# Optimization experiments

Measured on AMD Instinct MI355X. Metric: run time of the kernel, lower is better.

## Reference

```python
import jax, jax.numpy as jnp
import numpy as np
from itertools import combinations

BASIS = 16  # identity + sums over every nonempty subset of the 4 set axes


def eq4_layer(x, coefs, bias):
    """Permutation-equivariant 4->4 set layer.
    x: (B, Din, n, n, n, n); coefs: (Din, Dout, 16); bias: (Dout,)
    Basis op 0 is identity; ops 1..15 are sums over each nonempty subset of the
    four set axes, broadcast back to full shape. We never stack the 16 full-size
    ops: pooled ops are contracted in their small (keepdims) form and broadcast-added.
    """
    out = jnp.einsum('ds,bdijkl->bsijkl', coefs[:, :, 0], x)
    b = 1
    for r in range(1, 5):
        for axes in combinations((2, 3, 4, 5), r):
            m = x.sum(axis=axes, keepdims=True)  # small marginal tensor
            out = out + jnp.einsum('ds,bd...->bs...', coefs[:, :, b], m)
            b += 1
    return out + bias.reshape(1, -1, 1, 1, 1, 1)


def setup_inputs() -> dict:
    key = jax.random.key(0)
    ks = jax.random.split(key, 9)
    B, n = 4, 24
    nembed, embed_dim, hid, out_dim = 1000, 15, 16, 16
    D = embed_dim + 1  # 16, = layers[0]
    s = 0.1
    return {
        'xcat': jax.random.randint(ks[0], (B, n), 0, nembed),
        'xfeat': jax.random.normal(ks[1], (B, n), dtype=jnp.float32),
        'embed': jax.random.normal(ks[2], (nembed, embed_dim), dtype=jnp.float32) * s,
        'coefs1': jax.random.normal(ks[3], (D, hid, BASIS), dtype=jnp.float32) * s,
        'bias1': jnp.zeros((hid,), dtype=jnp.float32),
        'coefs2': jax.random.normal(ks[4], (hid, out_dim, BASIS), dtype=jnp.float32) * s,
        'bias2': jnp.zeros((out_dim,), dtype=jnp.float32),
        'w_out': jax.random.normal(ks[5], (1, out_dim), dtype=jnp.float32) * s,
        'b_out': jnp.zeros((1,), dtype=jnp.float32),
    }


def reference(xcat, xfeat, embed, coefs1, bias1, coefs2, bias2, w_out, b_out):
    e = jax.nn.relu(embed[xcat])                       # (B, n, embed_dim)
    x = jnp.concatenate([e, xfeat[..., None]], axis=-1)  # (B, n, D)
    # 4th-order outer product per channel: (B, D, n, n, n, n)
    T = jnp.einsum('bid,bjd,bkd,bld->bdijkl', x, x, x, x)
    T = jax.nn.relu(eq4_layer(T, coefs1, bias1))
    T = jax.nn.relu(eq4_layer(T, coefs2, bias2))
    pooled = T.sum(axis=(2, 3, 4, 5))                  # (B, out_dim)
    return pooled @ w_out.T + b_out                    # (B, 1)
```

## Files before the change

### kernel.cpp

```cpp
#include <hip/hip_runtime.h>
#include <hip/hip_bf16.h>


#define NB 4
#define NN 24
#define ND 16
#define NS 16
#define NO 16
#define NKL 576
#define TSTRIDE 1152

typedef unsigned int u32;
typedef unsigned short u16;

__device__ __forceinline__ u16 f2bf(float f) {
  u32 u = __float_as_uint(f);
  u = (u + 0x7fffu + ((u >> 16) & 1u)) >> 16;
  return (u16)u;
}
__device__ __forceinline__ float bflo(u32 u) { return __uint_as_float(u << 16); }
__device__ __forceinline__ float bfhi(u32 u) { return __uint_as_float(u & 0xffff0000u); }

__global__ __launch_bounds__(192, 2) void kb_eval(
    const int* __restrict__ xcat, const float* __restrict__ xfeat,
    const float* __restrict__ embed,
    const float* __restrict__ coefs1, const float* __restrict__ bias1,
    const float* __restrict__ coefs2,
    u32* __restrict__ T1g, u32* __restrict__ mkc_p, u32* __restrict__ mlc_p,
    u32* __restrict__ mklc_p) {
  const int blk = blockIdx.x;
  const int j = blk % NN, i = (blk / NN) % NN, b = blk / (NN * NN);
  const int t = threadIdx.x;
  __shared__ float sx[NN * ND];
  __shared__ float SwL[16];
  __shared__ float Af[256], tb[256], tg[256], td[256];
  __shared__ float dconst[16];
  __shared__ __align__(16) float tabL[TSTRIDE];
  __shared__ u32 T1p[NKL][9];
  __shared__ __align__(16) float rk[NN][20], rl[NN][20];
  __shared__ __align__(16) float rkl[16];
  __shared__ __align__(16) float c2kT[16][20], c2lT[16][20], c2qT[16][20];

  for (int idx = t; idx < NN * ND; idx += 192) {
    int d = idx & 15, ii = idx >> 4;
    float v;
    if (d < 15) v = fmaxf(embed[xcat[b * NN + ii] * 15 + d], 0.f);
    else        v = xfeat[b * NN + ii];
    sx[idx] = v;
  }
  for (int idx = t; idx < 256; idx += 192) {
    int s = idx >> 4, s2 = idx & 15;
    c2kT[s2][s] = coefs2[idx * 16 + 3];
    c2lT[s2][s] = coefs2[idx * 16 + 4];
    c2qT[s2][s] = coefs2[idx * 16 + 10];
  }
  __syncthreads();
  if (t < 16) {
    float s = 0.f;
    for (int ii = 0; ii < NN; ++ii) s += sx[ii * 16 + t];
    SwL[t] = s;
  }
  __syncthreads();
  for (int idx = t; idx < 256; idx += 192) {
    int d = idx >> 4, s = idx & 15;
    const float* c = coefs1 + idx * 16;
    float xi = sx[i * 16 + d], xj = sx[j * 16 + d];
    float Sv = SwL[d];
    float S2 = Sv * Sv, S3 = S2 * Sv, S4 = S2 * S2, pij = xi * xj;
    Af[s * 16 + d] = c[0] * pij + c[1] * Sv * xj + c[2] * Sv * xi + c[5] * S2;
    tb[idx] = c[4] * Sv * pij + c[9] * S2 * xi + c[7] * S2 * xj + c[12] * S3;
    tg[idx] = c[3] * Sv * pij + c[8] * S2 * xi + c[6] * S2 * xj + c[11] * S3;
    td[idx] = c[10] * S2 * pij + c[14] * S3 * xi + c[13] * S3 * xj + c[15] * S4;
  }
  __syncthreads();
  if (t < 16) {
    float sd = 0.f;
    for (int d = 0; d < 16; ++d) sd += td[d * 16 + t];
    dconst[t] = sd + bias1[t];
  }
  __syncthreads();
  if (t < 128) {
    int s = t >> 3, m = t & 7;
    tabL[t] = __uint_as_float((u32)f2bf(Af[s * 16 + 2 * m]) |
                              ((u32)f2bf(Af[s * 16 + 2 * m + 1]) << 16));
  }
  for (int idx = t; idx < 768; idx += 192) {
    int pos = idx >> 4, s = idx & 15;
    if (pos < NN) {
      float acc = 0.f;
#pragma unroll
      for (int d = 0; d < 16; ++d) acc += tb[d * 16 + s] * sx[pos * 16 + d];
      tabL[128 + s * 32 + (pos / 3) * 4 + pos % 3] = acc;
    } else {
      int l = pos - NN;
      float acc = dconst[s];
#pragma unroll
      for (int d = 0; d < 16; ++d) acc += tg[d * 16 + s] * sx[l * 16 + d];
      tabL[640 + s * 32 + (l / 3) * 4 + l % 3] = acc;
    }
  }
  __syncthreads();

  const int grp = t >> 3, sub = t & 7, vr = 3 * sub;
  const int grpPos = (grp / 3) * 4 + grp % 3;
  float P0[16], P1[16], P2[16];
#pragma unroll
  for (int d = 0; d < 16; ++d) {
    float xc = sx[grp * 16 + d];
    P0[d] = sx[vr * 16 + d] * xc;
    P1[d] = sx[(vr + 1) * 16 + d] * xc;
    P2[d] = sx[(vr + 2) * 16 + d] * xc;
  }
  float pr0[16], pr1[16], pr2[16];
#pragma unroll
  for (int s = 0; s < 16; ++s) {
    const uint4* ap = (const uint4*)(tabL + s * 8);
    uint4 A0 = ap[0], A1 = ap[1];
    u32 qa[8] = {A0.x, A0.y, A0.z, A0.w, A1.x, A1.y, A1.z, A1.w};
    float Afr[16];
#pragma unroll
    for (int m = 0; m < 8; ++m) {
      Afr[2 * m] = bflo(qa[m]);
      Afr[2 * m + 1] = bfhi(qa[m]);
    }
    float4 vb4 = *(const float4*)(tabL + 128 + s * 32 + sub * 4);
    float ct = tabL[640 + s * 32 + grpPos];
    float v0 = vb4.x + ct, v1 = vb4.y + ct, v2 = vb4.z + ct;
#pragma unroll
    for (int d = 0; d < 16; ++d) {
      v0 += Afr[d] * P0[d];
      v1 += Afr[d] * P1[d];
      v2 += Afr[d] * P2[d];
    }
    pr0[s] = fmaxf(v0, 0.f);
    pr1[s] = fmaxf(v1, 0.f);
    pr2[s] = fmaxf(v2, 0.f);
  }
  const int klA = vr * NN + grp;
  auto emit = [&](float (&pr)[16], int kl) {
    u32 w[8];
#pragma unroll
    for (int m = 0; m < 8; ++m) {
      w[m] = (u32)f2bf(pr[2 * m]) | ((u32)f2bf(pr[2 * m + 1]) << 16);
      T1p[kl][m] = w[m];
    }
    uint4* gp = (uint4*)(T1g + ((size_t)blk * NKL + kl) * 8);
    gp[0] = make_uint4(w[0], w[1], w[2], w[3]);
    gp[1] = make_uint4(w[4], w[5], w[6], w[7]);
  };
  emit(pr0, klA); emit(pr1, klA + NN); emit(pr2, klA + 2 * NN);
  __syncthreads();

  for (int idx = t; idx < NN * NS; idx += 192) {
    int a = idx >> 4, s = idx & 15, m = s >> 1;
    u32 odd = (u32)(s & 1);
    float sk = 0.f, sl = 0.f;
    for (int c = 0; c < NN; ++c) {
      u32 uk = T1p[c * NN + a][m];
      u32 ul = T1p[a * NN + c][m];
      sk += odd ? bfhi(uk) : bflo(uk);
      sl += odd ? bfhi(ul) : bflo(ul);
    }
    rk[a][s] = sk;
    rl[a][s] = sl;
  }
  __syncthreads();
  if (t < 16) {
    float v = 0.f;
    for (int a = 0; a < NN; ++a) v += rk[a][t];
    rkl[t] = v;
  }
  __syncthreads();
  for (int idx = t; idx < 392; idx += 192) {
    int m = idx & 7, pos = idx >> 3;
    const float* raw; const float (*cT)[20]; u32* dst;
    if (pos < NN)           { raw = rk[pos];      cT = c2kT; dst = mkc_p + ((size_t)blk * NN + pos) * 8 + m; }
    else if (pos < 2 * NN)  { raw = rl[pos - NN]; cT = c2lT; dst = mlc_p + ((size_t)blk * NN + (pos - NN)) * 8 + m; }
    else                    { raw = rkl;          cT = c2qT; dst = mklc_p + (size_t)blk * 8 + m; }
    float o0 = 0.f, o1 = 0.f;
#pragma unroll
    for (int w = 0; w < 4; ++w) {
      float4 rv = ((const float4*)raw)[w];
      float4 m0 = ((const float4*)(&cT[2 * m][0]))[w];
      float4 m1 = ((const float4*)(&cT[2 * m + 1][0]))[w];
      o0 += rv.x * m0.x + rv.y * m0.y + rv.z * m0.z + rv.w * m0.w;
      o1 += rv.x * m1.x + rv.y * m1.y + rv.z * m1.z + rv.w * m1.w;
    }
    *dst = (u32)f2bf(o0) | ((u32)f2bf(o1) << 16);
  }
}

__global__ __launch_bounds__(256) void k3_marg(
    const u32* __restrict__ T1g, const float* __restrict__ coefs2,
    u32* __restrict__ mi_p, u32* __restrict__ mj_p,
    u32* __restrict__ mic_p, u32* __restrict__ mjc_p,
    float* __restrict__ quad_part) {
  const int t = threadIdx.x, bb = blockIdx.x;
  const int pos = bb * 256 + t;
  const bool isI = pos < 55296;
  const int p = isI ? pos : pos - 55296;
  __shared__ __align__(16) float ccT[16][20];
  __shared__ float qred[4][16];
  {
    int s = t >> 4, s2 = t & 15;
    ccT[s2][s] = coefs2[t * 16 + (isI ? 1 : 2)];
  }
  __syncthreads();
  const int ba = p / NKL, kl = p % NKL;
  const int b = ba / NN, a = ba % NN;
  const u32* base; size_t stride;
  if (isI) { base = T1g + ((size_t)(b * NN * NN + a) * NKL + kl) * 8; stride = (size_t)NN * NKL * 8; }
  else     { base = T1g + ((size_t)((b * NN + a) * NN) * NKL + kl) * 8; stride = (size_t)NKL * 8; }
  float raw[16];
#pragma unroll
  for (int s = 0; s < 16; ++s) raw[s] = 0.f;
  for (int c = 0; c < NN; ++c) {
    const uint4* q = (const uint4*)(base + c * stride);
    uint4 q0 = q[0], q1 = q[1];
    u32 qa[8] = {q0.x, q0.y, q0.z, q0.w, q1.x, q1.y, q1.z, q1.w};
#pragma unroll
    for (int m = 0; m < 8; ++m) {
      raw[2 * m] += bflo(qa[m]);
      raw[2 * m + 1] += bfhi(qa[m]);
    }
  }
  u32 rp[8], op[8];
#pragma unroll
  for (int m = 0; m < 8; ++m) {
    rp[m] = (u32)f2bf(raw[2 * m]) | ((u32)f2bf(raw[2 * m + 1]) << 16);
    float o0 = 0.f, o1 = 0.f;
#pragma unroll
    for (int w = 0; w < 4; ++w) {
      float4 m0 = ((const float4*)(&ccT[2 * m][0]))[w];
      float4 m1 = ((const float4*)(&ccT[2 * m + 1][0]))[w];
      o0 += m0.x * raw[4 * w] + m0.y * raw[4 * w + 1] + m0.z * raw[4 * w + 2] + m0.w * raw[4 * w + 3];
      o1 += m1.x * raw[4 * w] + m1.y * raw[4 * w + 1] + m1.z * raw[4 * w + 2] + m1.w * raw[4 * w + 3];
    }
    op[m] = (u32)f2bf(o0) | ((u32)f2bf(o1) << 16);
  }
  uint4* rdst = (uint4*)((isI ? mi_p : mj_p) + (size_t)p * 8);
  rdst[0] = make_uint4(rp[0], rp[1], rp[2], rp[3]);
  rdst[1] = make_uint4(rp[4], rp[5], rp[6], rp[7]);
  uint4* cdst = (uint4*)((isI ? mic_p : mjc_p) + (size_t)p * 8);
  cdst[0] = make_uint4(op[0], op[1], op[2], op[3]);
  cdst[1] = make_uint4(op[4], op[5], op[6], op[7]);
  if (isI) {
#pragma unroll
    for (int s = 0; s < 16; ++s) {
      float v = raw[s];
      for (int off = 32; off; off >>= 1) v += __shfl_xor(v, off, 64);
      raw[s] = v;
    }
    if ((t & 63) == 0) {
      int w = t >> 6;
#pragma unroll
      for (int s = 0; s < 16; ++s) qred[w][s] = raw[s];
    }
  }
  __syncthreads();
  if (isI && t < 16)
    quad_part[bb * 16 + t] = qred[0][t] + qred[1][t] + qred[2][t] + qred[3][t];
}

__global__ __launch_bounds__(256) void kd_derived(
    const u32* __restrict__ mi_p, const u32* __restrict__ mj_p,
    const float* __restrict__ quad_part, const float* __restrict__ coefs2,
    float* __restrict__ mijc, float* __restrict__ mikc, float* __restrict__ milc,
    float* __restrict__ mjkc, float* __restrict__ mjlc,
    float* __restrict__ mijkc, float* __restrict__ mijlc,
    float* __restrict__ miklc, float* __restrict__ mjklc,
    float* __restrict__ mijklc) {
  const int bb = blockIdx.x, t = threadIdx.x;
  __shared__ float cc[256];
  __shared__ float ex[32][17];
  __shared__ float tot[16];
  __shared__ float qr[64];
  if (bb < 360) {
    int tbl = bb / 72;
    cc[t] = coefs2[t * 16 + 5 + tbl];
    int pp = t >> 3, m = t & 7;
    int pos = (bb % 72) * 32 + pp;
    int b = pos / 576, rem = pos % 576;
    const u32* srcb; int stride;
    if (tbl == 0) { srcb = mi_p + ((size_t)b * 24 * 576 + rem) * 8 + m; stride = 576 * 8; }
    else if (tbl == 1) { int jj = rem / 24, l = rem % 24;
      srcb = mi_p + (((size_t)(b * 24 + jj)) * 576 + l) * 8 + m; stride = 24 * 8; }
    else if (tbl == 2) { int jj = rem / 24, k = rem % 24;
      srcb = mi_p + (((size_t)(b * 24 + jj)) * 576 + k * 24) * 8 + m; stride = 8; }
    else if (tbl == 3) { int ii = rem / 24, l = rem % 24;
      srcb = mj_p + (((size_t)(b * 24 + ii)) * 576 + l) * 8 + m; stride = 24 * 8; }
    else { int ii = rem / 24, k = rem % 24;
      srcb = mj_p + (((size_t)(b * 24 + ii)) * 576 + k * 24) * 8 + m; stride = 8; }
    float v0 = 0.f, v1 = 0.f;
#pragma unroll 4
    for (int x = 0; x < 24; ++x) {
      u32 u = srcb[(size_t)x * stride];
      v0 += bflo(u); v1 += bfhi(u);
    }
    ex[pp][2 * m] = v0;
    ex[pp][2 * m + 1] = v1;
    __syncthreads();
    float* dst = (tbl == 0 ? mijc : tbl == 1 ? mikc : tbl == 2 ? milc : tbl == 3 ? mjkc : mjlc);
    for (int idx = t; idx < 512; idx += 256) {
      int pp2 = idx >> 4, s2 = idx & 15;
      float o = 0.f;
#pragma unroll
      for (int ss = 0; ss < 16; ++ss) o += cc[ss * 16 + s2] * ex[pp2][ss];
      dst[(size_t)((bb % 72) * 32 + pp2) * 16 + s2] = o;
    }
    return;
  }
  if (bb < 360 + 384) {
    int idx = bb - 360;
    int tbl = idx / 96, rr = idx % 96;
    int b = rr / 24, a = rr % 24;
    cc[t] = coefs2[t * 16 + 11 + tbl];
    int gg = t >> 3, m = t & 7;
    const u32* src = (tbl == 3 ? mj_p : mi_p);
    float v0 = 0.f, v1 = 0.f;
#pragma unroll 2
    for (int it = 0; it < 18; ++it) {
      int u = gg + (it << 5);
      size_t addr;
      if (tbl == 0) { int j = u / 24, k = u % 24;
        addr = (((size_t)(b * 24 + j)) * 576 + k * 24 + a) * 8 + m; }
      else if (tbl == 1) { int j = u / 24, l = u % 24;
        addr = (((size_t)(b * 24 + j)) * 576 + a * 24 + l) * 8 + m; }
      else {
        addr = (((size_t)(b * 24 + a)) * 576 + u) * 8 + m; }
      u32 uu = src[addr];
      v0 += bflo(uu); v1 += bfhi(uu);
    }
    ex[gg][2 * m] = v0;
    ex[gg][2 * m + 1] = v1;
    __syncthreads();
    if (t < 16) {
      float w2 = 0.f;
#pragma unroll
      for (int g2 = 0; g2 < 32; ++g2) w2 += ex[g2][t];
      tot[t] = w2;
    }
    __syncthreads();
    if (t < 16) {
      float o = 0.f;
#pragma unroll
      for (int ss = 0; ss < 16; ++ss) o += cc[ss * 16 + t] * tot[ss];
      float* dst = (tbl == 0 ? mijkc : tbl == 1 ? mijlc : tbl == 2 ? miklc : mjklc);
      dst[(size_t)(b * 24 + a) * 16 + t] = o;
    }
    return;
  }
  if (t < 64) {
    int b = t >> 4, s = t & 15;
    float v = 0.f;
    for (int c = 0; c < 54; ++c) v += quad_part[(b * 54 + c) * 16 + s];
    qr[t] = v;
  }
  __syncthreads();
  if (t < 64) {
    int b = t >> 4, s2 = t & 15;
    float o = 0.f;
#pragma unroll
    for (int s = 0; s < 16; ++s) o += coefs2[(s * 16 + s2) * 16 + 15] * qr[b * 16 + s];
    mijklc[t] = o;
  }
}

__global__ __launch_bounds__(192, 2) void k5_final(
    const u32* __restrict__ T1g,
    const u32* __restrict__ mic_p, const u32* __restrict__ mjc_p,
    const u32* __restrict__ mkc_p, const u32* __restrict__ mlc_p,
    const u32* __restrict__ mklc_p,
    const float* __restrict__ mijc, const float* __restrict__ mikc,
    const float* __restrict__ milc, const float* __restrict__ mjkc,
    const float* __restrict__ mjlc,
    const float* __restrict__ mijkc, const float* __restrict__ mijlc,
    const float* __restrict__ miklc, const float* __restrict__ mjklc,
    const float* __restrict__ mijklc,
    const float* __restrict__ coefs2, const float* __restrict__ bias2,
    const float* __restrict__ w_out, float* __restrict__ pool_part) {
  const int orig = blockIdx.x;
  const int blk = (orig & 7) * 288 + (orig >> 3);
  const int j = blk % NN, i2 = (blk / NN) % NN, b = blk / (NN * NN);
  const int t = threadIdx.x;
  __shared__ __align__(16) u32 c2p[128];
  __shared__ __align__(16) float Kt[NN][16], Lt[NN][16];
  __shared__ __align__(16) float cterm[16], wl[16];
  __shared__ float wsum[3];

  if (t < 128) {
    int s = t >> 3, m = t & 7;
    c2p[t] = (u32)f2bf(coefs2[(s * 16 + 2 * m) * 16]) |
             ((u32)f2bf(coefs2[(s * 16 + 2 * m + 1) * 16]) << 16);
  }
  for (int idx = t; idx < NN * NO; idx += 192) {
    int kk = idx >> 4, s2 = idx & 15, m = s2 >> 1;
    u32 odd = (u32)(s2 & 1);
    u32 ul = mlc_p[((size_t)blk * NN + kk) * 8 + m];
    u32 uk = mkc_p[((size_t)blk * NN + kk) * 8 + m];
    Kt[kk][s2] = (odd ? bfhi(ul) : bflo(ul))
               + mjlc[(size_t)((b * NN + i2) * NN + kk) * NS + s2]
               + milc[(size_t)((b * NN + j) * NN + kk) * NS + s2]
               + mijlc[(size_t)(b * NN + kk) * NS + s2];
    Lt[kk][s2] = (odd ? bfhi(uk) : bflo(uk))
               + mjkc[(size_t)((b * NN + i2) * NN + kk) * NS + s2]
               + mikc[(size_t)((b * NN + j) * NN + kk) * NS + s2]
               + mijkc[(size_t)(b * NN + kk) * NS + s2];
  }
  if (t < NO) {
    u32 uq = mklc_p[(size_t)blk * 8 + (t >> 1)];
    cterm[t] = ((t & 1) ? bfhi(uq) : bflo(uq))
             + miklc[(size_t)(b * NN + j) * NS + t]
             + mjklc[(size_t)(b * NN + i2) * NS + t]
             + mijklc[(size_t)b * NS + t] + bias2[t];
    wl[t] = w_out[t];
  }
  __syncthreads();

  u32 qa0[8], qa1[8], qa2[8];
  float acc0[16], acc1[16], acc2[16];
  auto loadElem = [&](int c, u32 (&qa)[8], float (&acc)[16]) {
    const int kl = t + 192 * c;
    const int k = kl / NN, l = kl % NN;
    const uint4* pt = (const uint4*)(T1g + ((size_t)blk * NKL + kl) * 8);
    const uint4* pi = (const uint4*)(mic_p + ((size_t)((b * NN + j) * NKL + kl)) * 8);
    const uint4* pj = (const uint4*)(mjc_p + ((size_t)((b * NN + i2) * NKL + kl)) * 8);
    const float4* ps = (const float4*)(mijc + ((size_t)(b * NKL + kl)) * 16);
    uint4 t0 = pt[0], t1 = pt[1];
    uint4 i0 = pi[0], i1 = pi[1];
    uint4 j0 = pj[0], j1 = pj[1];
    float4 s0 = ps[0], s1 = ps[1], s2v = ps[2], s3 = ps[3];
    qa[0] = t0.x; qa[1] = t0.y; qa[2] = t0.z; qa[3] = t0.w;
    qa[4] = t1.x; qa[5] = t1.y; qa[6] = t1.z; qa[7] = t1.w;
    u32 ia[8] = {i0.x, i0.y, i0.z, i0.w, i1.x, i1.y, i1.z, i1.w};
    u32 ja[8] = {j0.x, j0.y, j0.z, j0.w, j1.x, j1.y, j1.z, j1.w};
    float sv[16];
    ((float4*)sv)[0] = s0; ((float4*)sv)[1] = s1; ((float4*)sv)[2] = s2v; ((float4*)sv)[3] = s3;
#pragma unroll
    for (int m = 0; m < 8; ++m) {
      acc[2 * m]     = cterm[2 * m]     + Kt[k][2 * m]     + Lt[l][2 * m]
                     + bflo(ia[m]) + bflo(ja[m]) + sv[2 * m];
      acc[2 * m + 1] = cterm[2 * m + 1] + Kt[k][2 * m + 1] + Lt[l][2 * m + 1]
                     + bfhi(ia[m]) + bfhi(ja[m]) + sv[2 * m + 1];
    }
  };
  loadElem(0, qa0, acc0); loadElem(1, qa1, acc1); loadElem(2, qa2, acc2);

#pragma unroll
  for (int s = 0; s < 16; ++s) {
    const uint4* cp = (const uint4*)(c2p + s * 8);
    uint4 C0 = cp[0], C1 = cp[1];
    u32 ca[8] = {C0.x, C0.y, C0.z, C0.w, C1.x, C1.y, C1.z, C1.w};
    float row[16];
#pragma unroll
    for (int m = 0; m < 8; ++m) {
      row[2 * m] = bflo(ca[m]);
      row[2 * m + 1] = bfhi(ca[m]);
    }
    float v0 = (s & 1) ? bfhi(qa0[s >> 1]) : bflo(qa0[s >> 1]);
    float v1 = (s & 1) ? bfhi(qa1[s >> 1]) : bflo(qa1[s >> 1]);
    float v2 = (s & 1) ? bfhi(qa2[s >> 1]) : bflo(qa2[s >> 1]);
#pragma unroll
    for (int s2 = 0; s2 < 16; ++s2) {
      acc0[s2] += row[s2] * v0;
      acc1[s2] += row[s2] * v1;
      acc2[s2] += row[s2] * v2;
    }
  }
  float p = 0.f;
#pragma unroll
  for (int s2 = 0; s2 < 16; ++s2)
    p += wl[s2] * (fmaxf(acc0[s2], 0.f) + fmaxf(acc1[s2], 0.f) + fmaxf(acc2[s2], 0.f));
  for (int off = 32; off; off >>= 1) p += __shfl_down(p, off, 64);
  if ((t & 63) == 0) wsum[t >> 6] = p;
  __syncthreads();
  if (t == 0) pool_part[blk] = wsum[0] + wsum[1] + wsum[2];
}

__global__ __launch_bounds__(256) void k6_out(
    const float* __restrict__ pool_part, const float* __restrict__ b_out,
    float* __restrict__ out) {
  const int t = threadIdx.x;
  const int b = t >> 6, lane = t & 63;
  float v = 0.f;
  for (int c = lane; c < 576; c += 64) v += pool_part[b * 576 + c];
  for (int off = 32; off; off >>= 1) v += __shfl_down(v, off, 64);
  if (lane == 0) out[b] = v + b_out[0];
}

extern "C" void kernel_launch(void* const* d_in, const int* in_sizes, int n_in,
                              void* d_out, int out_size, void* d_ws, size_t ws_size,
                              hipStream_t stream) {
  (void)in_sizes; (void)n_in; (void)out_size; (void)ws_size;
  const int*   xcat   = (const int*)d_in[0];
  const float* xfeat  = (const float*)d_in[1];
  const float* embed  = (const float*)d_in[2];
  const float* coefs1 = (const float*)d_in[3];
  const float* bias1  = (const float*)d_in[4];
  const float* coefs2 = (const float*)d_in[5];
  const float* bias2  = (const float*)d_in[6];
  const float* w_out  = (const float*)d_in[7];
  const float* b_out  = (const float*)d_in[8];
  float* out = (float*)d_out;
  char* ws = (char*)d_ws;

  u32*   T1g      = (u32*)(ws + 0);
  u32*   mi_p     = (u32*)(ws + 42467328);
  u32*   mj_p     = (u32*)(ws + 44236800);
  u32*   mic_p    = (u32*)(ws + 46006272);
  u32*   mjc_p    = (u32*)(ws + 47775744);
  u32*   mkc_p    = (u32*)(ws + 49545216);
  u32*   mlc_p    = (u32*)(ws + 51314688);
  u32*   mklc_p   = (u32*)(ws + 53084160);
  float* mijc     = (float*)(ws + 53157888);
  float* mikc     = (float*)(ws + 53305344);
  float* milc     = (float*)(ws + 53452800);
  float* mjkc     = (float*)(ws + 53600256);
  float* mjlc     = (float*)(ws + 53747712);
  float* mijkc    = (float*)(ws + 53895168);
  float* mijlc    = (float*)(ws + 53901312);
  float* miklc    = (float*)(ws + 53907456);
  float* mjklc    = (float*)(ws + 53913600);
  float* mijklc   = (float*)(ws + 53919744);
  float* quad_part= (float*)(ws + 53920000);
  float* pool_part= (float*)(ws + 53933824);

  kb_eval<<<NB * NN * NN, 192, 0, stream>>>(xcat, xfeat, embed, coefs1, bias1,
                                            coefs2, T1g, mkc_p, mlc_p, mklc_p);
  k3_marg<<<432, 256, 0, stream>>>(T1g, coefs2, mi_p, mj_p, mic_p, mjc_p, quad_part);
  kd_derived<<<745, 256, 0, stream>>>(mi_p, mj_p, quad_part, coefs2,
                                      mijc, mikc, milc, mjkc, mjlc,
                                      mijkc, mijlc, miklc, mjklc, mijklc);
  k5_final<<<NB * NN * NN, 192, 0, stream>>>(T1g, mic_p, mjc_p, mkc_p, mlc_p, mklc_p,
                                             mijc, mikc, milc, mjkc, mjlc,
                                             mijkc, mijlc, miklc, mjklc, mijklc,
                                             coefs2, bias2, w_out, pool_part);
  k6_out<<<1, 256, 0, stream>>>(pool_part, b_out, out);
}
```

Baseline: 101.3 us.

## Move per-block k/l marginal reductions from kb_eval into k5_final

The k- and l-axis marginal sums of T1, and their contraction with coefs2, now happen in k5_final instead of kb_eval. k5_final already loads the block's T1 tile, so the mkc/mlc/mklc intermediate buffers and their global writes and reads disappear. kb_eval becomes lighter: fewer shared arrays, fewer barriers, the A table computed straight from coefs1, the dconst reduction folded into the tg loop, and T1 packed to bf16 on the fly. This moves reduction work, shared memory and barriers into k5_final, which may lower its occupancy. It also adds an unroll pragma in k3_marg.

```diff
diff --git a/kernel.cpp b/kernel.cpp
--- a/kernel.cpp
+++ b/kernel.cpp
@@ -8,7 +8,6 @@
 #define NS 16
 #define NO 16
 #define NKL 576
-#define TSTRIDE 1152
 
 typedef unsigned int u32;
 typedef unsigned short u16;
@@ -25,21 +24,14 @@
     const int* __restrict__ xcat, const float* __restrict__ xfeat,
     const float* __restrict__ embed,
     const float* __restrict__ coefs1, const float* __restrict__ bias1,
-    const float* __restrict__ coefs2,
-    u32* __restrict__ T1g, u32* __restrict__ mkc_p, u32* __restrict__ mlc_p,
-    u32* __restrict__ mklc_p) {
+    u32* __restrict__ T1g) {
   const int blk = blockIdx.x;
   const int j = blk % NN, i = (blk / NN) % NN, b = blk / (NN * NN);
   const int t = threadIdx.x;
   __shared__ float sx[NN * ND];
   __shared__ float SwL[16];
-  __shared__ float Af[256], tb[256], tg[256], td[256];
-  __shared__ float dconst[16];
-  __shared__ __align__(16) float tabL[TSTRIDE];
-  __shared__ u32 T1p[NKL][9];
-  __shared__ __align__(16) float rk[NN][20], rl[NN][20];
-  __shared__ __align__(16) float rkl[16];
-  __shared__ __align__(16) float c2kT[16][20], c2lT[16][20], c2qT[16][20];
+  __shared__ float tb[256], tg[256], td[256];
+  __shared__ __align__(16) float tabL[1152];
 
   for (int idx = t; idx < NN * ND; idx += 192) {
     int d = idx & 15, ii = idx >> 4;
@@ -48,12 +40,6 @@
     else        v = xfeat[b * NN + ii];
     sx[idx] = v;
   }
-  for (int idx = t; idx < 256; idx += 192) {
-    int s = idx >> 4, s2 = idx & 15;
-    c2kT[s2][s] = coefs2[idx * 16 + 3];
-    c2lT[s2][s] = coefs2[idx * 16 + 4];
-    c2qT[s2][s] = coefs2[idx * 16 + 10];
-  }
   __syncthreads();
   if (t < 16) {
     float s = 0.f;
@@ -67,23 +53,24 @@
     float xi = sx[i * 16 + d], xj = sx[j * 16 + d];
     float Sv = SwL[d];
     float S2 = Sv * Sv, S3 = S2 * Sv, S4 = S2 * S2, pij = xi * xj;
-    Af[s * 16 + d] = c[0] * pij + c[1] * Sv * xj + c[2] * Sv * xi + c[5] * S2;
     tb[idx] = c[4] * Sv * pij + c[9] * S2 * xi + c[7] * S2 * xj + c[12] * S3;
     tg[idx] = c[3] * Sv * pij + c[8] * S2 * xi + c[6] * S2 * xj + c[11] * S3;
     td[idx] = c[10] * S2 * pij + c[14] * S3 * xi + c[13] * S3 * xj + c[15] * S4;
   }
-  __syncthreads();
-  if (t < 16) {
-    float sd = 0.f;
-    for (int d = 0; d < 16; ++d) sd += td[d * 16 + t];
-    dconst[t] = sd + bias1[t];
-  }
-  __syncthreads();
   if (t < 128) {
     int s = t >> 3, m = t & 7;
-    tabL[t] = __uint_as_float((u32)f2bf(Af[s * 16 + 2 * m]) |
-                              ((u32)f2bf(Af[s * 16 + 2 * m + 1]) << 16));
-  }
+    float af[2];
+#pragma unroll
+    for (int h = 0; h < 2; ++h) {
+      int d = 2 * m + h;
+      const float* c = coefs1 + (d * 16 + s) * 16;
+      float xi = sx[i * 16 + d], xj = sx[j * 16 + d];
+      float Sv = SwL[d];
+      af[h] = c[0] * xi * xj + c[1] * Sv * xj + c[2] * Sv * xi + c[5] * Sv * Sv;
+    }
+    tabL[t] = __uint_as_float((u32)f2bf(af[0]) | ((u32)f2bf(af[1]) << 16));
+  }
+  __syncthreads();
   for (int idx = t; idx < 768; idx += 192) {
     int pos = idx >> 4, s = idx & 15;
     if (pos < NN) {
@@ -93,14 +80,14 @@
       tabL[128 + s * 32 + (pos / 3) * 4 + pos % 3] = acc;
     } else {
       int l = pos - NN;
-      float acc = dconst[s];
-#pragma unroll
-      for (int d = 0; d < 16; ++d) acc += tg[d * 16 + s] * sx[l * 16 + d];
+      float acc = bias1[s];
+#pragma unroll
+      for (int d = 0; d < 16; ++d)
+        acc += tg[d * 16 + s] * sx[l * 16 + d] + td[d * 16 + s];
       tabL[640 + s * 32 + (l / 3) * 4 + l % 3] = acc;
     }
   }
   __syncthreads();
-
   const int grp = t >> 3, sub = t & 7, vr = 3 * sub;
   const int grpPos = (grp / 3) * 4 + grp % 3;
   float P0[16], P1[16], P2[16];
@@ -111,7 +98,7 @@
     P1[d] = sx[(vr + 1) * 16 + d] * xc;
     P2[d] = sx[(vr + 2) * 16 + d] * xc;
   }
-  float pr0[16], pr1[16], pr2[16];
+  u32 w0[8], w1[8], w2[8];
 #pragma unroll
   for (int s = 0; s < 16; ++s) {
     const uint4* ap = (const uint4*)(tabL + s * 8);
@@ -132,62 +119,18 @@
       v1 += Afr[d] * P1[d];
       v2 += Afr[d] * P2[d];
     }
-    pr0[s] = fmaxf(v0, 0.f);
-    pr1[s] = fmaxf(v1, 0.f);
-    pr2[s] = fmaxf(v2, 0.f);
+    v0 = fmaxf(v0, 0.f); v1 = fmaxf(v1, 0.f); v2 = fmaxf(v2, 0.f);
+    u16 b0 = f2bf(v0), b1 = f2bf(v1), b2 = f2bf(v2);
+    if (s & 1) { w0[s >> 1] |= (u32)b0 << 16; w1[s >> 1] |= (u32)b1 << 16; w2[s >> 1] |= (u32)b2 << 16; }
+    else       { w0[s >> 1] = b0; w1[s >> 1] = b1; w2[s >> 1] = b2; }
   }
   const int klA = vr * NN + grp;
-  auto emit = [&](float (&pr)[16], int kl) {
-    u32 w[8];
-#pragma unroll
-    for (int m = 0; m < 8; ++m) {
-      w[m] = (u32)f2bf(pr[2 * m]) | ((u32)f2bf(pr[2 * m + 1]) << 16);
-      T1p[kl][m] = w[m];
-    }
+  auto emit = [&](u32 (&w)[8], int kl) {
     uint4* gp = (uint4*)(T1g + ((size_t)blk * NKL + kl) * 8);
     gp[0] = make_uint4(w[0], w[1], w[2], w[3]);
     gp[1] = make_uint4(w[4], w[5], w[6], w[7]);
   };
-  emit(pr0, klA); emit(pr1, klA + NN); emit(pr2, klA + 2 * NN);
-  __syncthreads();
-
-  for (int idx = t; idx < NN * NS; idx += 192) {
-    int a = idx >> 4, s = idx & 15, m = s >> 1;
-    u32 odd = (u32)(s & 1);
-    float sk = 0.f, sl = 0.f;
-    for (int c = 0; c < NN; ++c) {
-      u32 uk = T1p[c * NN + a][m];
-      u32 ul = T1p[a * NN + c][m];
-      sk += odd ? bfhi(uk) : bflo(uk);
-      sl += odd ? bfhi(ul) : bflo(ul);
-    }
-    rk[a][s] = sk;
-    rl[a][s] = sl;
-  }
-  __syncthreads();
-  if (t < 16) {
-    float v = 0.f;
-    for (int a = 0; a < NN; ++a) v += rk[a][t];
-    rkl[t] = v;
-  }
-  __syncthreads();
-  for (int idx = t; idx < 392; idx += 192) {
-    int m = idx & 7, pos = idx >> 3;
-    const float* raw; const float (*cT)[20]; u32* dst;
-    if (pos < NN)           { raw = rk[pos];      cT = c2kT; dst = mkc_p + ((size_t)blk * NN + pos) * 8 + m; }
-    else if (pos < 2 * NN)  { raw = rl[pos - NN]; cT = c2lT; dst = mlc_p + ((size_t)blk * NN + (pos - NN)) * 8 + m; }
-    else                    { raw = rkl;          cT = c2qT; dst = mklc_p + (size_t)blk * 8 + m; }
-    float o0 = 0.f, o1 = 0.f;
-#pragma unroll
-    for (int w = 0; w < 4; ++w) {
-      float4 rv = ((const float4*)raw)[w];
-      float4 m0 = ((const float4*)(&cT[2 * m][0]))[w];
-      float4 m1 = ((const float4*)(&cT[2 * m + 1][0]))[w];
-      o0 += rv.x * m0.x + rv.y * m0.y + rv.z * m0.z + rv.w * m0.w;
-      o1 += rv.x * m1.x + rv.y * m1.y + rv.z * m1.z + rv.w * m1.w;
-    }
-    *dst = (u32)f2bf(o0) | ((u32)f2bf(o1) << 16);
-  }
+  emit(w0, klA); emit(w1, klA + NN); emit(w2, klA + 2 * NN);
 }
 
 __global__ __launch_bounds__(256) void k3_marg(
@@ -214,6 +157,7 @@
   float raw[16];
 #pragma unroll
   for (int s = 0; s < 16; ++s) raw[s] = 0.f;
+#pragma unroll 4
   for (int c = 0; c < NN; ++c) {
     const uint4* q = (const uint4*)(base + c * stride);
     uint4 q0 = q[0], q1 = q[1];
@@ -369,8 +313,6 @@
 __global__ __launch_bounds__(192, 2) void k5_final(
     const u32* __restrict__ T1g,
     const u32* __restrict__ mic_p, const u32* __restrict__ mjc_p,
-    const u32* __restrict__ mkc_p, const u32* __restrict__ mlc_p,
-    const u32* __restrict__ mklc_p,
     const float* __restrict__ mijc, const float* __restrict__ mikc,
     const float* __restrict__ milc, const float* __restrict__ mjkc,
     const float* __restrict__ mjlc,
@@ -384,32 +326,85 @@
   const int j = blk % NN, i2 = (blk / NN) % NN, b = blk / (NN * NN);
   const int t = threadIdx.x;
   __shared__ __align__(16) u32 c2p[128];
+  __shared__ __align__(16) float c2kT[16][20], c2lT[16][20], c2qT[16][20];
+  __shared__ u32 T1p[NKL][9];
+  __shared__ __align__(16) float rk[NN][20], rl[NN][20];
+  __shared__ __align__(16) float rkl[16];
   __shared__ __align__(16) float Kt[NN][16], Lt[NN][16];
   __shared__ __align__(16) float cterm[16], wl[16];
   __shared__ float wsum[3];
 
+  u32 qa0[8], qa1[8], qa2[8];
+  auto loadT = [&](int c, u32 (&qa)[8]) {
+    const int kl = t + 192 * c;
+    const uint4* pt = (const uint4*)(T1g + ((size_t)blk * NKL + kl) * 8);
+    uint4 t0 = pt[0], t1 = pt[1];
+    qa[0] = t0.x; qa[1] = t0.y; qa[2] = t0.z; qa[3] = t0.w;
+    qa[4] = t1.x; qa[5] = t1.y; qa[6] = t1.z; qa[7] = t1.w;
+#pragma unroll
+    for (int m = 0; m < 8; ++m) T1p[kl][m] = qa[m];
+  };
+  loadT(0, qa0); loadT(1, qa1); loadT(2, qa2);
   if (t < 128) {
     int s = t >> 3, m = t & 7;
     c2p[t] = (u32)f2bf(coefs2[(s * 16 + 2 * m) * 16]) |
              ((u32)f2bf(coefs2[(s * 16 + 2 * m + 1) * 16]) << 16);
   }
+  for (int idx = t; idx < 256; idx += 192) {
+    int s = idx >> 4, s2 = idx & 15;
+    c2kT[s2][s] = coefs2[idx * 16 + 3];
+    c2lT[s2][s] = coefs2[idx * 16 + 4];
+    c2qT[s2][s] = coefs2[idx * 16 + 10];
+  }
+  __syncthreads();
+
+  for (int idx = t; idx < NN * NS; idx += 192) {
+    int a = idx >> 4, s = idx & 15, m = s >> 1;
+    u32 odd = (u32)(s & 1);
+    float sk = 0.f, sl = 0.f;
+    for (int c = 0; c < NN; ++c) {
+      u32 uk = T1p[c * NN + a][m];
+      u32 ul = T1p[a * NN + c][m];
+      sk += odd ? bfhi(uk) : bflo(uk);
+      sl += odd ? bfhi(ul) : bflo(ul);
+    }
+    rk[a][s] = sk;
+    rl[a][s] = sl;
+  }
+  __syncthreads();
+  if (t < 16) {
+    float v = 0.f;
+    for (int a = 0; a < NN; ++a) v += rk[a][t];
+    rkl[t] = v;
+  }
+  __syncthreads();
   for (int idx = t; idx < NN * NO; idx += 192) {
-    int kk = idx >> 4, s2 = idx & 15, m = s2 >> 1;
-    u32 odd = (u32)(s2 & 1);
-    u32 ul = mlc_p[((size_t)blk * NN + kk) * 8 + m];
-    u32 uk = mkc_p[((size_t)blk * NN + kk) * 8 + m];
-    Kt[kk][s2] = (odd ? bfhi(ul) : bflo(ul))
+    int kk = idx >> 4, s2 = idx & 15;
+    const float4* ck = (const float4*)(&c2kT[s2][0]);
+    const float4* cl = (const float4*)(&c2lT[s2][0]);
+    const float4* rkr = (const float4*)(&rk[kk][0]);
+    const float4* rlr = (const float4*)(&rl[kk][0]);
+    float ok = 0.f, ol = 0.f;
+#pragma unroll
+    for (int w = 0; w < 4; ++w) {
+      float4 mk4 = ck[w], ml4 = cl[w], rk4 = rkr[w], rl4 = rlr[w];
+      ok += mk4.x * rk4.x + mk4.y * rk4.y + mk4.z * rk4.z + mk4.w * rk4.w;
+      ol += ml4.x * rl4.x + ml4.y * rl4.y + ml4.z * rl4.z + ml4.w * rl4.w;
+    }
+    Lt[kk][s2] = ok
+               + mjkc[(size_t)((b * NN + i2) * NN + kk) * NS + s2]
+               + mikc[(size_t)((b * NN + j) * NN + kk) * NS + s2]
+               + mijkc[(size_t)(b * NN + kk) * NS + s2];
+    Kt[kk][s2] = ol
                + mjlc[(size_t)((b * NN + i2) * NN + kk) * NS + s2]
                + milc[(size_t)((b * NN + j) * NN + kk) * NS + s2]
                + mijlc[(size_t)(b * NN + kk) * NS + s2];
-    Lt[kk][s2] = (odd ? bfhi(uk) : bflo(uk))
-               + mjkc[(size_t)((b * NN + i2) * NN + kk) * NS + s2]
-               + mikc[(size_t)((b * NN + j) * NN + kk) * NS + s2]
-               + mijkc[(size_t)(b * NN + kk) * NS + s2];
   }
   if (t < NO) {
-    u32 uq = mklc_p[(size_t)blk * 8 + (t >> 1)];
-    cterm[t] = ((t & 1) ? bfhi(uq) : bflo(uq))
+    float oq = 0.f;
+#pragma unroll
+    for (int s = 0; s < 16; ++s) oq += c2qT[t][s] * rkl[s];
+    cterm[t] = oq
              + miklc[(size_t)(b * NN + j) * NS + t]
              + mjklc[(size_t)(b * NN + i2) * NS + t]
              + mijklc[(size_t)b * NS + t] + bias2[t];
@@ -417,21 +412,16 @@
   }
   __syncthreads();
 
-  u32 qa0[8], qa1[8], qa2[8];
   float acc0[16], acc1[16], acc2[16];
-  auto loadElem = [&](int c, u32 (&qa)[8], float (&acc)[16]) {
+  auto initElem = [&](int c, u32 (&qa)[8], float (&acc)[16]) {
     const int kl = t + 192 * c;
     const int k = kl / NN, l = kl % NN;
-    const uint4* pt = (const uint4*)(T1g + ((size_t)blk * NKL + kl) * 8);
     const uint4* pi = (const uint4*)(mic_p + ((size_t)((b * NN + j) * NKL + kl)) * 8);
     const uint4* pj = (const uint4*)(mjc_p + ((size_t)((b * NN + i2) * NKL + kl)) * 8);
     const float4* ps = (const float4*)(mijc + ((size_t)(b * NKL + kl)) * 16);
-    uint4 t0 = pt[0], t1 = pt[1];
     uint4 i0 = pi[0], i1 = pi[1];
     uint4 j0 = pj[0], j1 = pj[1];
     float4 s0 = ps[0], s1 = ps[1], s2v = ps[2], s3 = ps[3];
-    qa[0] = t0.x; qa[1] = t0.y; qa[2] = t0.z; qa[3] = t0.w;
-    qa[4] = t1.x; qa[5] = t1.y; qa[6] = t1.z; qa[7] = t1.w;
     u32 ia[8] = {i0.x, i0.y, i0.z, i0.w, i1.x, i1.y, i1.z, i1.w};
     u32 ja[8] = {j0.x, j0.y, j0.z, j0.w, j1.x, j1.y, j1.z, j1.w};
     float sv[16];
@@ -444,7 +434,7 @@
                      + bfhi(ia[m]) + bfhi(ja[m]) + sv[2 * m + 1];
     }
   };
-  loadElem(0, qa0, acc0); loadElem(1, qa1, acc1); loadElem(2, qa2, acc2);
+  initElem(0, qa0, acc0); initElem(1, qa1, acc1); initElem(2, qa2, acc2);
 
 #pragma unroll
   for (int s = 0; s < 16; ++s) {
@@ -509,29 +499,25 @@
   u32*   mj_p     = (u32*)(ws + 44236800);
   u32*   mic_p    = (u32*)(ws + 46006272);
   u32*   mjc_p    = (u32*)(ws + 47775744);
-  u32*   mkc_p    = (u32*)(ws + 49545216);
-  u32*   mlc_p    = (u32*)(ws + 51314688);
-  u32*   mklc_p   = (u32*)(ws + 53084160);
-  float* mijc     = (float*)(ws + 53157888);
-  float* mikc     = (float*)(ws + 53305344);
-  float* milc     = (float*)(ws + 53452800);
-  float* mjkc     = (float*)(ws + 53600256);
-  float* mjlc     = (float*)(ws + 53747712);
-  float* mijkc    = (float*)(ws + 53895168);
-  float* mijlc    = (float*)(ws + 53901312);
-  float* miklc    = (float*)(ws + 53907456);
-  float* mjklc    = (float*)(ws + 53913600);
-  float* mijklc   = (float*)(ws + 53919744);
-  float* quad_part= (float*)(ws + 53920000);
-  float* pool_part= (float*)(ws + 53933824);
-
-  kb_eval<<<NB * NN * NN, 192, 0, stream>>>(xcat, xfeat, embed, coefs1, bias1,
-                                            coefs2, T1g, mkc_p, mlc_p, mklc_p);
+  float* mijc     = (float*)(ws + 49545216);
+  float* mikc     = (float*)(ws + 49692672);
+  float* milc     = (float*)(ws + 49840128);
+  float* mjkc     = (float*)(ws + 49987584);
+  float* mjlc     = (float*)(ws + 50135040);
+  float* mijkc    = (float*)(ws + 50282496);
+  float* mijlc    = (float*)(ws + 50288640);
+  float* miklc    = (float*)(ws + 50294784);
+  float* mjklc    = (float*)(ws + 50300928);
+  float* mijklc   = (float*)(ws + 50307072);
+  float* quad_part= (float*)(ws + 50307328);
+  float* pool_part= (float*)(ws + 50321152);
+
+  kb_eval<<<NB * NN * NN, 192, 0, stream>>>(xcat, xfeat, embed, coefs1, bias1, T1g);
   k3_marg<<<432, 256, 0, stream>>>(T1g, coefs2, mi_p, mj_p, mic_p, mjc_p, quad_part);
   kd_derived<<<745, 256, 0, stream>>>(mi_p, mj_p, quad_part, coefs2,
                                       mijc, mikc, milc, mjkc, mjlc,
                                       mijkc, mijlc, miklc, mjklc, mijklc);
-  k5_final<<<NB * NN * NN, 192, 0, stream>>>(T1g, mic_p, mjc_p, mkc_p, mlc_p, mklc_p,
+  k5_final<<<NB * NN * NN, 192, 0, stream>>>(T1g, mic_p, mjc_p,
                                              mijc, mikc, milc, mjkc, mjlc,
                                              mijkc, mijlc, miklc, mjklc, mijklc,
                                              coefs2, bias2, w_out, pool_part);
```

After: 169.0 us. +66.9%, slower.
